# Optimization experiments

Measured on AMD Instinct MI355X. Metric: run time of the kernel, lower is better.

## Reference

```python
import jax, jax.numpy as jnp
import numpy as np
import math

B, T, C = 2, 2048, 1024
N_HEADS = 16  # config.head_size in the original (actually number of heads)
HEAD_DIM = C // N_HEADS


def setup_inputs() -> dict:
    key = jax.random.key(0)
    k1, k2, k3 = jax.random.split(key, 3)
    s = 1.0 / math.sqrt(C)
    return {
        "x": jax.random.normal(k1, (B, T, C), dtype=jnp.float32),
        "W_attn": jax.random.normal(k2, (C, 3 * C), dtype=jnp.float32) * s,
        "b_attn": jnp.zeros((3 * C,), dtype=jnp.float32),
        "W_proj": jax.random.normal(k3, (C, C), dtype=jnp.float32) * s,
        "b_proj": jnp.zeros((C,), dtype=jnp.float32),
    }


def reference(x, W_attn, b_attn, W_proj, b_proj):
    Bsz, Tlen, Cdim = x.shape
    qkv = x @ W_attn + b_attn                      # [B,T,3C]
    q, k, v = jnp.split(qkv, 3, axis=-1)
    # [B,T,C] -> [B,H,T,D]
    def to_heads(t):
        return t.reshape(Bsz, Tlen, N_HEADS, HEAD_DIM).transpose(0, 2, 1, 3)
    q, k, v = to_heads(q), to_heads(k), to_heads(v)
    # NOTE: original multiplies by sqrt(head_dim) (faithful to source, not 1/sqrt)
    scale = jnp.asarray(math.sqrt(HEAD_DIM), dtype=x.dtype)
    att = jnp.einsum("bhqd,bhkd->bhqk", q, k) * scale
    causal = jnp.tril(jnp.ones((Tlen, Tlen), dtype=bool))
    att = jnp.where(causal[None, None, :, :], att, jnp.asarray(-jnp.inf, x.dtype))
    att = jax.nn.softmax(att, axis=-1)
    # dropout layers are identity in eval mode
    y = jnp.einsum("bhqk,bhkd->bhqd", att, v)
    y = y.transpose(0, 2, 1, 3).reshape(Bsz, Tlen, Cdim)
    return y @ W_proj + b_proj
```

## Files before the change

### kernel.cpp

```cpp
#include <hip/hip_runtime.h>
#include <hip/hip_bf16.h>


#define B_  2
#define T_  2048
#define C_  1024
#define H_  16
#define D_  64
#define M_  (B_ * T_)
#define N3_ (3 * C_)

typedef __attribute__((ext_vector_type(8))) short s16x8;
typedef __attribute__((ext_vector_type(4))) short s16x4;
typedef __attribute__((ext_vector_type(4))) float f32x4;

typedef const __attribute__((address_space(1))) unsigned int gu32_t;
typedef __attribute__((address_space(3))) unsigned int lu32_t;

#define MFMA16(a, b, c) __builtin_amdgcn_mfma_f32_16x16x32_bf16(a, b, c, 0, 0, 0)

__device__ __forceinline__ void gload_lds16(const short* g, short* l) {
    __builtin_amdgcn_global_load_lds((gu32_t*)g, (lu32_t*)l, 16, 0, 0);
}

__device__ __forceinline__ float b2f(unsigned short u) {
    return __uint_as_float(((unsigned)u) << 16);
}
__device__ __forceinline__ unsigned short f2b(float f) {
    unsigned u = __float_as_uint(f);
    return (unsigned short)((u + 0x7FFFu + ((u >> 16) & 1u)) >> 16);
}
__device__ __forceinline__ float fexp2(float x) {
#if __has_builtin(__builtin_amdgcn_exp2f)
    return __builtin_amdgcn_exp2f(x);
#else
    return exp2f(x);
#endif
}

__global__ __launch_bounds__(256) void cvt_all(
    const float* __restrict__ x,  short* __restrict__ xh,   short* __restrict__ xl,
    const float* __restrict__ Wa, short* __restrict__ WaTh, short* __restrict__ WaTl,
    const float* __restrict__ Wp, short* __restrict__ WpT)
{
    __shared__ short th[64][80];
    __shared__ short tl[64][80];
    const int tid = threadIdx.x;
    const int bid = blockIdx.x;

    if (bid < 2048) {
        int i = (bid * 256 + tid) * 8;
        float4 a = *(const float4*)&x[i];
        float4 b = *(const float4*)&x[i + 4];
        float v[8] = {a.x, a.y, a.z, a.w, b.x, b.y, b.z, b.w};
        s16x8 h, l;
        #pragma unroll
        for (int j = 0; j < 8; j++) {
            unsigned short hb = f2b(v[j]);
            h[j] = (short)hb;
            l[j] = (short)f2b(v[j] - b2f(hb));
        }
        *(s16x8*)&xh[i] = h;
        *(s16x8*)&xl[i] = l;
        return;
    }

    if (bid < 2816) {
        int r  = bid - 2048;
        int bx = r % 48, by = r / 48;
        const int k0 = by * 64, n0 = bx * 64;
        const int R = C_, Cn = N3_;
        {
            int rl = tid >> 4, cl = (tid & 15) * 4;
            #pragma unroll
            for (int i = 0; i < 4; i++) {
                int kr = rl + i * 16;
                float4 v4 = *(const float4*)&Wa[(size_t)(k0 + kr) * Cn + n0 + cl];
                float v[4] = {v4.x, v4.y, v4.z, v4.w};
                #pragma unroll
                for (int j = 0; j < 4; j++) {
                    unsigned short hb = f2b(v[j]);
                    th[cl + j][kr] = (short)hb;
                    tl[cl + j][kr] = (short)f2b(v[j] - b2f(hb));
                }
            }
        }
        __syncthreads();
        {
            int ro = tid >> 2, co = (tid & 3) * 16;
            *(s16x8*)&WaTh[(size_t)(n0 + ro) * R + k0 + co]     = *(s16x8*)&th[ro][co];
            *(s16x8*)&WaTh[(size_t)(n0 + ro) * R + k0 + co + 8] = *(s16x8*)&th[ro][co + 8];
            *(s16x8*)&WaTl[(size_t)(n0 + ro) * R + k0 + co]     = *(s16x8*)&tl[ro][co];
            *(s16x8*)&WaTl[(size_t)(n0 + ro) * R + k0 + co + 8] = *(s16x8*)&tl[ro][co + 8];
        }
        return;
    }

    {
        int r  = bid - 2816;
        int bx = r & 15, by = r >> 4;
        const int k0 = by * 64, n0 = bx * 64;
        const int R = C_, Cn = C_;
        {
            int rl = tid >> 4, cl = (tid & 15) * 4;
            #pragma unroll
            for (int i = 0; i < 4; i++) {
                int kr = rl + i * 16;
                float4 v = *(const float4*)&Wp[(size_t)(k0 + kr) * Cn + n0 + cl];
                th[cl + 0][kr] = (short)f2b(v.x);
                th[cl + 1][kr] = (short)f2b(v.y);
                th[cl + 2][kr] = (short)f2b(v.z);
                th[cl + 3][kr] = (short)f2b(v.w);
            }
        }
        __syncthreads();
        {
            int ro = tid >> 2, co = (tid & 3) * 16;
            *(s16x8*)&WpT[(size_t)(n0 + ro) * R + k0 + co]     = *(s16x8*)&th[ro][co];
            *(s16x8*)&WpT[(size_t)(n0 + ro) * R + k0 + co + 8] = *(s16x8*)&th[ro][co + 8];
        }
    }
}

__global__ __launch_bounds__(256) void qkv_qk(
    const short* __restrict__ Ah, const short* __restrict__ Al,
    const short* __restrict__ BTh, const short* __restrict__ BTl,
    const float* __restrict__ bias,
    short* __restrict__ Qh, short* __restrict__ Ql,
    short* __restrict__ Kh, short* __restrict__ Kl)
{
    __shared__ short Ash[2][128 * 32], Asl[2][128 * 32];
    __shared__ short Bsh[2][128 * 32], Bsl[2][128 * 32];

    const int tid  = threadIdx.x;
    const int wave = tid >> 6, lane = tid & 63;
    const int wm = wave >> 1, wn = wave & 1;
    const int lm = lane & 15, lq = lane >> 4;
    const int fid = blockIdx.y * 16 + blockIdx.x;
    const int wg  = (fid & 7) * 64 + (fid >> 3);
    const int n0  = (wg & 15) * 128;
    const int m0  = (wg >> 4) * 128;
    const int gr  = (lane >> 2);
    const int gc  = (((lane & 3) ^ ((lane >> 3) & 3)) << 3);
    const int sg  = ((lq ^ ((lm >> 1) & 3)) << 3);

    f32x4 acc[4][4] = {};

    for (int k0 = 0; k0 < C_; k0 += 64) {
        __syncthreads();
        #pragma unroll
        for (int p = 0; p < 2; p++) {
            int kp = k0 + p * 32;
            #pragma unroll
            for (int j = 0; j < 2; j++) {
                int s = wave * 2 + j;
                int row = s * 16 + gr;
                size_t ga = (size_t)(m0 + row) * C_ + kp + gc;
                size_t gb = (size_t)(n0 + row) * C_ + kp + gc;
                gload_lds16(&Ah[ga],  &Ash[p][s * 512]);
                gload_lds16(&Al[ga],  &Asl[p][s * 512]);
                gload_lds16(&BTh[gb], &Bsh[p][s * 512]);
                gload_lds16(&BTl[gb], &Bsl[p][s * 512]);
            }
        }
        __syncthreads();

        #pragma unroll
        for (int p = 0; p < 2; p++) {
            s16x8 ah[4], al[4], bh[4], bl[4];
            #pragma unroll
            for (int mi = 0; mi < 4; mi++) {
                int r = wm * 64 + mi * 16 + lm;
                ah[mi] = *(const s16x8*)&Ash[p][r * 32 + sg];
                al[mi] = *(const s16x8*)&Asl[p][r * 32 + sg];
            }
            #pragma unroll
            for (int nj = 0; nj < 4; nj++) {
                int r = wn * 64 + nj * 16 + lm;
                bh[nj] = *(const s16x8*)&Bsh[p][r * 32 + sg];
                bl[nj] = *(const s16x8*)&Bsl[p][r * 32 + sg];
            }
            #pragma unroll
            for (int mi = 0; mi < 4; mi++)
                #pragma unroll
                for (int nj = 0; nj < 4; nj++) {
                    acc[mi][nj] = MFMA16(ah[mi], bh[nj], acc[mi][nj]);
                    acc[mi][nj] = MFMA16(ah[mi], bl[nj], acc[mi][nj]);
                    acc[mi][nj] = MFMA16(al[mi], bh[nj], acc[mi][nj]);
                }
        }
    }

    #pragma unroll
    for (int nj = 0; nj < 4; nj++) {
        int n = n0 + wn * 64 + nj * 16 + lm;
        float bv = bias[n];
        int isK = n >> 10;
        int c = n & (C_ - 1);
        int h = c >> 6, d = c & (D_ - 1);
        short* dh = isK ? Kh : Qh;
        short* dl = isK ? Kl : Ql;
        float scale = isK ? 1.0f : 11.541560327111708f;
        #pragma unroll
        for (int mi = 0; mi < 4; mi++) {
            #pragma unroll
            for (int r = 0; r < 4; r++) {
                int m  = m0 + wm * 64 + mi * 16 + lq * 4 + r;
                int bb = m >> 11, t = m & (T_ - 1);
                float v = (acc[mi][nj][r] + bv) * scale;
                size_t idx = (((size_t)bb * H_ + h) * T_ + t) * D_ + d;
                unsigned short hb = f2b(v);
                dh[idx] = (short)hb;
                dl[idx] = (short)f2b(v - b2f(hb));
            }
        }
    }
}

__global__ __launch_bounds__(256, 4) void qkv_v(
    const short* __restrict__ Ah, const short* __restrict__ BTh,
    const float* __restrict__ bias, short* __restrict__ VT)
{
    __shared__ short Ash[2][64 * 32];
    __shared__ short Bsh[2][128 * 32];

    const int tid  = threadIdx.x;
    const int wave = tid >> 6, lane = tid & 63;
    const int wm = wave >> 1, wn = wave & 1;
    const int lm = lane & 15, lq = lane >> 4;
    const int fid = blockIdx.y * 8 + blockIdx.x;
    const int wg  = (fid & 7) * 64 + (fid >> 3);
    const int n0  = (wg & 7) * 128;
    const int m0  = (wg >> 3) * 64;
    const int gr  = (lane >> 2);
    const int gc  = (((lane & 3) ^ ((lane >> 3) & 3)) << 3);
    const int sg  = ((lq ^ ((lm >> 1) & 3)) << 3);

    f32x4 acc[2][4] = {};

    for (int k0 = 0; k0 < C_; k0 += 64) {
        __syncthreads();
        #pragma unroll
        for (int p = 0; p < 2; p++) {
            int kp = k0 + p * 32;
            int rowA = wave * 16 + gr;
            gload_lds16(&Ah[(size_t)(m0 + rowA) * C_ + kp + gc], &Ash[p][wave * 512]);
            #pragma unroll
            for (int j = 0; j < 2; j++) {
                int s = wave * 2 + j;
                int rowB = s * 16 + gr;
                gload_lds16(&BTh[(size_t)(n0 + rowB) * C_ + kp + gc], &Bsh[p][s * 512]);
            }
        }
        __syncthreads();

        #pragma unroll
        for (int p = 0; p < 2; p++) {
            s16x8 af[2], bfr[4];
            #pragma unroll
            for (int mi = 0; mi < 2; mi++)
                af[mi] = *(const s16x8*)&Ash[p][(wm * 32 + mi * 16 + lm) * 32 + sg];
            #pragma unroll
            for (int nj = 0; nj < 4; nj++)
                bfr[nj] = *(const s16x8*)&Bsh[p][(wn * 64 + nj * 16 + lm) * 32 + sg];
            #pragma unroll
            for (int mi = 0; mi < 2; mi++)
                #pragma unroll
                for (int nj = 0; nj < 4; nj++)
                    acc[mi][nj] = MFMA16(af[mi], bfr[nj], acc[mi][nj]);
        }
    }

    #pragma unroll
    for (int nj = 0; nj < 4; nj++) {
        int n = n0 + wn * 64 + nj * 16 + lm;
        float bv = bias[n];
        int h = n >> 6, d = n & (D_ - 1);
        #pragma unroll
        for (int mi = 0; mi < 2; mi++) {
            #pragma unroll
            for (int r = 0; r < 4; r++) {
                int m  = m0 + wm * 32 + mi * 16 + lq * 4 + r;
                int bb = m >> 11, t = m & (T_ - 1);
                VT[(((size_t)bb * H_ + h) * D_ + d) * T_ + t] =
                    (short)f2b(acc[mi][nj][r] + bv);
            }
        }
    }
}

__global__ __launch_bounds__(256, 4) void proj_mfma(
    const short* __restrict__ Ah, const short* __restrict__ BTh,
    const float* __restrict__ bias, float* __restrict__ out)
{
    __shared__ short Ash[2][64 * 32];
    __shared__ short Bsh[2][128 * 32];

    const int tid  = threadIdx.x;
    const int wave = tid >> 6, lane = tid & 63;
    const int wm = wave >> 1, wn = wave & 1;
    const int lm = lane & 15, lq = lane >> 4;
    const int fid = blockIdx.y * 8 + blockIdx.x;
    const int wg  = (fid & 7) * 64 + (fid >> 3);
    const int n0  = (wg & 7) * 128;
    const int m0  = (wg >> 3) * 64;
    const int gr  = (lane >> 2);
    const int gc  = (((lane & 3) ^ ((lane >> 3) & 3)) << 3);
    const int sg  = ((lq ^ ((lm >> 1) & 3)) << 3);

    f32x4 acc[2][4] = {};

    for (int k0 = 0; k0 < C_; k0 += 64) {
        __syncthreads();
        #pragma unroll
        for (int p = 0; p < 2; p++) {
            int kp = k0 + p * 32;
            int rowA = wave * 16 + gr;
            gload_lds16(&Ah[(size_t)(m0 + rowA) * C_ + kp + gc], &Ash[p][wave * 512]);
            #pragma unroll
            for (int j = 0; j < 2; j++) {
                int s = wave * 2 + j;
                int rowB = s * 16 + gr;
                gload_lds16(&BTh[(size_t)(n0 + rowB) * C_ + kp + gc], &Bsh[p][s * 512]);
            }
        }
        __syncthreads();

        #pragma unroll
        for (int p = 0; p < 2; p++) {
            s16x8 af[2], bfr[4];
            #pragma unroll
            for (int mi = 0; mi < 2; mi++)
                af[mi] = *(const s16x8*)&Ash[p][(wm * 32 + mi * 16 + lm) * 32 + sg];
            #pragma unroll
            for (int nj = 0; nj < 4; nj++)
                bfr[nj] = *(const s16x8*)&Bsh[p][(wn * 64 + nj * 16 + lm) * 32 + sg];
            #pragma unroll
            for (int mi = 0; mi < 2; mi++)
                #pragma unroll
                for (int nj = 0; nj < 4; nj++)
                    acc[mi][nj] = MFMA16(af[mi], bfr[nj], acc[mi][nj]);
        }
    }

    #pragma unroll
    for (int nj = 0; nj < 4; nj++) {
        int n = n0 + wn * 64 + nj * 16 + lm;
        float bv = bias[n];
        #pragma unroll
        for (int mi = 0; mi < 2; mi++) {
            #pragma unroll
            for (int r = 0; r < 4; r++) {
                int m = m0 + wm * 32 + mi * 16 + lq * 4 + r;
                out[(size_t)m * C_ + n] = acc[mi][nj][r] + bv;
            }
        }
    }
}

__device__ __forceinline__ void online_sm(
    f32x4 S[4], float& mrow, float& lrow, f32x4 O[4], int quad)
{
    float v[16];
    #pragma unroll
    for (int t = 0; t < 4; t++)
        #pragma unroll
        for (int r = 0; r < 4; r++) v[t * 4 + r] = S[t][r];
    #pragma unroll
    for (int s = 8; s; s >>= 1)
        #pragma unroll
        for (int i = 0; i < s; i++) v[i] = fmaxf(v[i], v[i + s]);
    float rm = v[0];
    rm = fmaxf(rm, __shfl_xor(rm, 16, 64));
    rm = fmaxf(rm, __shfl_xor(rm, 32, 64));
    if (!__all(rm - mrow <= 8.f)) {
        float mnew  = fmaxf(mrow, rm);
        float alpha = fexp2(mrow - mnew);
        mrow = mnew;
        lrow *= alpha;
        float al[4];
        #pragma unroll
        for (int r = 0; r < 4; r++) al[r] = __shfl(alpha, quad * 4 + r, 64);
        #pragma unroll
        for (int t = 0; t < 4; t++)
            #pragma unroll
            for (int r = 0; r < 4; r++) O[t][r] *= al[r];
    }
    float sv[16];
    #pragma unroll
    for (int t = 0; t < 4; t++)
        #pragma unroll
        for (int r = 0; r < 4; r++) {
            float p = fexp2(S[t][r] - mrow);
            S[t][r] = p;
            sv[t * 4 + r] = p;
        }
    #pragma unroll
    for (int s = 8; s; s >>= 1)
        #pragma unroll
        for (int i = 0; i < s; i++) sv[i] += sv[i + s];
    float rs = sv[0];
    rs += __shfl_xor(rs, 16, 64);
    rs += __shfl_xor(rs, 32, 64);
    lrow += rs;
}

__global__ __launch_bounds__(256, 2) void attn_mfma(
    const short* __restrict__ Qh, const short* __restrict__ Ql,
    const short* __restrict__ Kh, const short* __restrict__ Kl,
    const short* __restrict__ VT, short* __restrict__ Yb)
{
    __shared__ short Ksh[64][64], Ksl[64][64];
    __shared__ short Vt [64][64];
    __shared__ short Ps [4][2][16][64];

    const int tid  = threadIdx.x;
    const int wave = tid >> 6, lane = tid & 63;
    const int lm   = lane & 15, quad = lane >> 4;
    const int swz  = (lm & 7) << 3;

    const int bid = blockIdx.x;
    const int xcd = bid & 7;
    const int r_  = bid >> 3;
    const int bhl = r_ & 3;
    const int u   = r_ >> 2;
    const int g_  = u >> 3, j_ = u & 7;
    const int j   = g_ ? (15 - j_) : j_;
    const int bh  = xcd * 4 + bhl;
    const int b   = bh >> 4, h = bh & (H_ - 1);
    const int qtA = j, qtB = 31 - j;
    const int q0A = qtA * 64, q0B = qtB * 64;
    const size_t base  = (size_t)bh * T_ * D_;
    const size_t vbase = (size_t)bh * D_ * T_;

    const int src = tid >> 3;
    const int sch = (tid & 7) * 8;
    const int wsw = sch ^ ((src & 7) << 3);

    s16x8 bqhA[2], bqlA[2], bqhB[2], bqlB[2];
    #pragma unroll
    for (int kc = 0; kc < 2; kc++) {
        size_t ga = base + (size_t)(q0A + wave * 16 + lm) * D_ + kc * 32 + quad * 8;
        size_t gb = base + (size_t)(q0B + wave * 16 + lm) * D_ + kc * 32 + quad * 8;
        bqhA[kc] = *(const s16x8*)&Qh[ga];
        bqlA[kc] = *(const s16x8*)&Ql[ga];
        bqhB[kc] = *(const s16x8*)&Qh[gb];
        bqlB[kc] = *(const s16x8*)&Ql[gb];
    }

    s16x8 pkh[2], pkl[2], pvt[2];
    #pragma unroll
    for (int i = 0; i < 2; i++) {
        int row = i * 32 + src;
        size_t gk = base + (size_t)row * D_ + sch;
        pkh[i] = *(const s16x8*)&Kh[gk];
        pkl[i] = *(const s16x8*)&Kl[gk];
        pvt[i] = *(const s16x8*)&VT[vbase + (size_t)row * T_ + sch];
    }

    float mA = -INFINITY, lA = 0.f;
    float mB = -INFINITY, lB = 0.f;
    f32x4 OA[4] = {}, OB[4] = {};

    for (int kt = 0; kt <= qtB; kt++) {
        __syncthreads();
        #pragma unroll
        for (int i = 0; i < 2; i++) {
            int row = i * 32 + src;
            *(s16x8*)&Ksh[row][wsw] = pkh[i];
            *(s16x8*)&Ksl[row][wsw] = pkl[i];
            *(s16x8*)&Vt [row][wsw] = pvt[i];
        }
        if (kt < qtB) {
            #pragma unroll
            for (int i = 0; i < 2; i++) {
                int row = i * 32 + src;
                size_t gk = base + (size_t)((kt + 1) * 64 + row) * D_ + sch;
                pkh[i] = *(const s16x8*)&Kh[gk];
                pkl[i] = *(const s16x8*)&Kl[gk];
                pvt[i] = *(const s16x8*)&VT[vbase + (size_t)row * T_ + (kt + 1) * 64 + sch];
            }
        }
        __syncthreads();

        const bool doA = (kt <= qtA);
        const int  qg  = wave * 16 + lm;

        f32x4 SB[4] = {}, SA[4] = {};
        if (doA) {
            #pragma unroll
            for (int t = 0; t < 4; t++)
                #pragma unroll
                for (int kc = 0; kc < 2; kc++) {
                    s16x8 kh8 = *(const s16x8*)&Ksh[t * 16 + lm][(kc * 32 + quad * 8) ^ swz];
                    s16x8 kl8 = *(const s16x8*)&Ksl[t * 16 + lm][(kc * 32 + quad * 8) ^ swz];
                    SB[t] = MFMA16(kh8, bqhB[kc], SB[t]);
                    SB[t] = MFMA16(kl8, bqhB[kc], SB[t]);
                    SB[t] = MFMA16(kh8, bqlB[kc], SB[t]);
                    SA[t] = MFMA16(kh8, bqhA[kc], SA[t]);
                    SA[t] = MFMA16(kl8, bqhA[kc], SA[t]);
                    SA[t] = MFMA16(kh8, bqlA[kc], SA[t]);
                }
        } else {
            #pragma unroll
            for (int t = 0; t < 4; t++)
                #pragma unroll
                for (int kc = 0; kc < 2; kc++) {
                    s16x8 kh8 = *(const s16x8*)&Ksh[t * 16 + lm][(kc * 32 + quad * 8) ^ swz];
                    s16x8 kl8 = *(const s16x8*)&Ksl[t * 16 + lm][(kc * 32 + quad * 8) ^ swz];
                    SB[t] = MFMA16(kh8, bqhB[kc], SB[t]);
                    SB[t] = MFMA16(kl8, bqhB[kc], SB[t]);
                    SB[t] = MFMA16(kh8, bqlB[kc], SB[t]);
                }
        }

        if (kt == qtB) {
            #pragma unroll
            for (int t = 0; t < 4; t++)
                #pragma unroll
                for (int r = 0; r < 4; r++)
                    if ((t * 16 + quad * 4 + r) > qg) SB[t][r] = -INFINITY;
        }
        if (kt == qtA) {
            #pragma unroll
            for (int t = 0; t < 4; t++)
                #pragma unroll
                for (int r = 0; r < 4; r++)
                    if ((t * 16 + quad * 4 + r) > qg) SA[t][r] = -INFINITY;
        }

        online_sm(SB, mB, lB, OB, quad);
        if (doA) online_sm(SA, mA, lA, OA, quad);

        #pragma unroll
        for (int t = 0; t < 4; t++) {
            s16x4 p;
            #pragma unroll
            for (int r = 0; r < 4; r++)
                p[r] = (short)(__float_as_uint(SB[t][r]) >> 16);
            *(s16x4*)&Ps[wave][0][lm][(t * 16 + quad * 4) ^ swz] = p;
        }
        if (doA) {
            #pragma unroll
            for (int t = 0; t < 4; t++) {
                s16x4 p;
                #pragma unroll
                for (int r = 0; r < 4; r++)
                    p[r] = (short)(__float_as_uint(SA[t][r]) >> 16);
                *(s16x4*)&Ps[wave][1][lm][(t * 16 + quad * 4) ^ swz] = p;
            }
        }

        s16x8 apB[2], apA[2];
        #pragma unroll
        for (int kc = 0; kc < 2; kc++)
            apB[kc] = *(const s16x8*)&Ps[wave][0][lm][(kc * 32 + quad * 8) ^ swz];
        if (doA) {
            #pragma unroll
            for (int kc = 0; kc < 2; kc++)
                apA[kc] = *(const s16x8*)&Ps[wave][1][lm][(kc * 32 + quad * 8) ^ swz];
            #pragma unroll
            for (int t = 0; t < 4; t++)
                #pragma unroll
                for (int kc = 0; kc < 2; kc++) {
                    s16x8 bv = *(const s16x8*)&Vt[t * 16 + lm][(kc * 32 + quad * 8) ^ swz];
                    OB[t] = MFMA16(apB[kc], bv, OB[t]);
                    OA[t] = MFMA16(apA[kc], bv, OA[t]);
                }
        } else {
            #pragma unroll
            for (int t = 0; t < 4; t++)
                #pragma unroll
                for (int kc = 0; kc < 2; kc++) {
                    s16x8 bv = *(const s16x8*)&Vt[t * 16 + lm][(kc * 32 + quad * 8) ^ swz];
                    OB[t] = MFMA16(apB[kc], bv, OB[t]);
                }
        }
    }

    float liA[4], liB[4];
    #pragma unroll
    for (int r = 0; r < 4; r++) {
        liA[r] = 1.0f / __shfl(lA, quad * 4 + r, 64);
        liB[r] = 1.0f / __shfl(lB, quad * 4 + r, 64);
    }
    #pragma unroll
    for (int t = 0; t < 4; t++)
        #pragma unroll
        for (int r = 0; r < 4; r++) {
            int d  = t * 16 + lm;
            int qa = q0A + wave * 16 + quad * 4 + r;
            int qb = q0B + wave * 16 + quad * 4 + r;
            Yb[((size_t)b * T_ + qa) * C_ + h * D_ + d] =
                (short)f2b(OA[t][r] * liA[r]);
            Yb[((size_t)b * T_ + qb) * C_ + h * D_ + d] =
                (short)f2b(OB[t][r] * liB[r]);
        }
}

extern "C" void kernel_launch(void* const* d_in, const int* in_sizes, int n_in,
                              void* d_out, int out_size, void* d_ws, size_t ws_size,
                              hipStream_t stream)
{
    const float* x      = (const float*)d_in[0];
    const float* W_attn = (const float*)d_in[1];
    const float* b_attn = (const float*)d_in[2];
    const float* W_proj = (const float*)d_in[3];
    const float* b_proj = (const float*)d_in[4];
    float* out = (float*)d_out;

    char* ws = (char*)d_ws;
    const size_t MB = 1024 * 1024;
    short* Qh   = (short*)(ws);
    short* Ql   = (short*)(ws +  8 * MB);
    short* Kh   = (short*)(ws + 16 * MB);
    short* Kl   = (short*)(ws + 24 * MB);
    short* xh   = (short*)(ws + 32 * MB);
    short* xl   = (short*)(ws + 40 * MB);
    short* WaTh = (short*)(ws + 48 * MB);
    short* WaTl = (short*)(ws + 54 * MB);
    short* WpT  = (short*)(ws + 60 * MB);
    short* VT   = (short*)(ws + 40 * MB);
    short* Yb   = (short*)(ws + 32 * MB);

    cvt_all<<<dim3(3072), 256, 0, stream>>>(x, xh, xl, W_attn, WaTh, WaTl,
                                            W_proj, WpT);

    qkv_qk <<<dim3(16, 32), 256, 0, stream>>>(xh, xl, WaTh, WaTl, b_attn,
                                              Qh, Ql, Kh, Kl);
    qkv_v  <<<dim3(8, 64), 256, 0, stream>>>(xh, WaTh + (size_t)2048 * C_,
                                             b_attn + 2048, VT);
    attn_mfma<<<dim3(512), 256, 0, stream>>>(Qh, Ql, Kh, Kl, VT, Yb);
    proj_mfma<<<dim3(8, 64), 256, 0, stream>>>(Yb, WpT, b_proj, out);
}
```

Before: 239.5 us.

## Double attention key tile to 128 keys per iteration

Each loop iteration of the attention kernel now processes 128 keys instead of 64. The K, K-low and V tiles in shared memory are enlarged to match, and the causal mask uses a half-tile threshold. This halves the loop trips, barriers and online-softmax rescale checks. In exchange it uses more LDS and registers, which may lower occupancy, and it computes extra masked work on the diagonal chunk when the query tile index is even.

```diff
diff --git a/kernel.cpp b/kernel.cpp
--- a/kernel.cpp
+++ b/kernel.cpp
@@ -358,19 +358,18 @@
     }
 }
 
-__device__ __forceinline__ void online_sm(
-    f32x4 S[4], float& mrow, float& lrow, f32x4 O[4], int quad)
+__device__ __forceinline__ void online_sm8(
+    f32x4 S[8], float& mrow, float& lrow, f32x4 O[4], int quad)
 {
-    float v[16];
-    #pragma unroll
-    for (int t = 0; t < 4; t++)
-        #pragma unroll
-        for (int r = 0; r < 4; r++) v[t * 4 + r] = S[t][r];
-    #pragma unroll
-    for (int s = 8; s; s >>= 1)
-        #pragma unroll
-        for (int i = 0; i < s; i++) v[i] = fmaxf(v[i], v[i + s]);
-    float rm = v[0];
+    float a[8];
+    #pragma unroll
+    for (int t = 0; t < 8; t++)
+        a[t] = fmaxf(fmaxf(S[t][0], S[t][1]), fmaxf(S[t][2], S[t][3]));
+    #pragma unroll
+    for (int s = 4; s; s >>= 1)
+        #pragma unroll
+        for (int i = 0; i < s; i++) a[i] = fmaxf(a[i], a[i + s]);
+    float rm = a[0];
     rm = fmaxf(rm, __shfl_xor(rm, 16, 64));
     rm = fmaxf(rm, __shfl_xor(rm, 32, 64));
     if (!__all(rm - mrow <= 8.f)) {
@@ -386,17 +385,15 @@
             #pragma unroll
             for (int r = 0; r < 4; r++) O[t][r] *= al[r];
     }
-    float sv[16];
-    #pragma unroll
-    for (int t = 0; t < 4; t++)
-        #pragma unroll
-        for (int r = 0; r < 4; r++) {
-            float p = fexp2(S[t][r] - mrow);
-            S[t][r] = p;
-            sv[t * 4 + r] = p;
-        }
-    #pragma unroll
-    for (int s = 8; s; s >>= 1)
+    float sv[8];
+    #pragma unroll
+    for (int t = 0; t < 8; t++) {
+        #pragma unroll
+        for (int r = 0; r < 4; r++) S[t][r] = fexp2(S[t][r] - mrow);
+        sv[t] = (S[t][0] + S[t][1]) + (S[t][2] + S[t][3]);
+    }
+    #pragma unroll
+    for (int s = 4; s; s >>= 1)
         #pragma unroll
         for (int i = 0; i < s; i++) sv[i] += sv[i + s];
     float rs = sv[0];
@@ -410,9 +407,9 @@
     const short* __restrict__ Kh, const short* __restrict__ Kl,
     const short* __restrict__ VT, short* __restrict__ Yb)
 {
-    __shared__ short Ksh[64][64], Ksl[64][64];
-    __shared__ short Vt [64][64];
-    __shared__ short Ps [4][2][16][64];
+    __shared__ short Ksh[128][64], Ksl[128][64];
+    __shared__ short Vt [64][128];
+    __shared__ short Ps [4][2][16][128];
 
     const int tid  = threadIdx.x;
     const int wave = tid >> 6, lane = tid & 63;
@@ -430,12 +427,11 @@
     const int b   = bh >> 4, h = bh & (H_ - 1);
     const int qtA = j, qtB = 31 - j;
     const int q0A = qtA * 64, q0B = qtB * 64;
+    const int cA  = qtA >> 1, cB = qtB >> 1;
+    const int thrA = (qtA & 1) << 6;
+    const int thrB = (qtB & 1) << 6;
     const size_t base  = (size_t)bh * T_ * D_;
     const size_t vbase = (size_t)bh * D_ * T_;
-
-    const int src = tid >> 3;
-    const int sch = (tid & 7) * 8;
-    const int wsw = sch ^ ((src & 7) << 3);
 
     s16x8 bqhA[2], bqlA[2], bqhB[2], bqlB[2];
     #pragma unroll
@@ -448,48 +444,56 @@
         bqlB[kc] = *(const s16x8*)&Ql[gb];
     }
 
-    s16x8 pkh[2], pkl[2], pvt[2];
-    #pragma unroll
-    for (int i = 0; i < 2; i++) {
-        int row = i * 32 + src;
-        size_t gk = base + (size_t)row * D_ + sch;
+    s16x8 pkh[4], pkl[4], pvt[4];
+    #pragma unroll
+    for (int i = 0; i < 4; i++) {
+        int g  = i * 256 + tid;
+        int rk = g >> 3, ck = (g & 7) * 8;
+        size_t gk = base + (size_t)rk * D_ + ck;
         pkh[i] = *(const s16x8*)&Kh[gk];
         pkl[i] = *(const s16x8*)&Kl[gk];
-        pvt[i] = *(const s16x8*)&VT[vbase + (size_t)row * T_ + sch];
+        int rv = g >> 4, cv = (g & 15) * 8;
+        pvt[i] = *(const s16x8*)&VT[vbase + (size_t)rv * T_ + cv];
     }
 
     float mA = -INFINITY, lA = 0.f;
     float mB = -INFINITY, lB = 0.f;
     f32x4 OA[4] = {}, OB[4] = {};
 
-    for (int kt = 0; kt <= qtB; kt++) {
-        __syncthreads();
-        #pragma unroll
-        for (int i = 0; i < 2; i++) {
-            int row = i * 32 + src;
-            *(s16x8*)&Ksh[row][wsw] = pkh[i];
-            *(s16x8*)&Ksl[row][wsw] = pkl[i];
-            *(s16x8*)&Vt [row][wsw] = pvt[i];
-        }
-        if (kt < qtB) {
-            #pragma unroll
-            for (int i = 0; i < 2; i++) {
-                int row = i * 32 + src;
-                size_t gk = base + (size_t)((kt + 1) * 64 + row) * D_ + sch;
+    for (int c = 0; c <= cB; c++) {
+        __syncthreads();
+        #pragma unroll
+        for (int i = 0; i < 4; i++) {
+            int g  = i * 256 + tid;
+            int rk = g >> 3;
+            int wK = ((g & 7) * 8) ^ ((rk & 7) << 3);
+            *(s16x8*)&Ksh[rk][wK] = pkh[i];
+            *(s16x8*)&Ksl[rk][wK] = pkl[i];
+            int rv = g >> 4;
+            int wV = ((g & 15) * 8) ^ ((rv & 7) << 3);
+            *(s16x8*)&Vt[rv][wV] = pvt[i];
+        }
+        if (c < cB) {
+            #pragma unroll
+            for (int i = 0; i < 4; i++) {
+                int g  = i * 256 + tid;
+                int rk = g >> 3, ck = (g & 7) * 8;
+                size_t gk = base + (size_t)((c + 1) * 128 + rk) * D_ + ck;
                 pkh[i] = *(const s16x8*)&Kh[gk];
                 pkl[i] = *(const s16x8*)&Kl[gk];
-                pvt[i] = *(const s16x8*)&VT[vbase + (size_t)row * T_ + (kt + 1) * 64 + sch];
-            }
-        }
-        __syncthreads();
-
-        const bool doA = (kt <= qtA);
+                int rv = g >> 4, cv = (g & 15) * 8;
+                pvt[i] = *(const s16x8*)&VT[vbase + (size_t)rv * T_ + (c + 1) * 128 + cv];
+            }
+        }
+        __syncthreads();
+
+        const bool doA = (c <= cA);
         const int  qg  = wave * 16 + lm;
 
-        f32x4 SB[4] = {}, SA[4] = {};
+        f32x4 SB[8] = {}, SA[8] = {};
         if (doA) {
             #pragma unroll
-            for (int t = 0; t < 4; t++)
+            for (int t = 0; t < 8; t++)
                 #pragma unroll
                 for (int kc = 0; kc < 2; kc++) {
                     s16x8 kh8 = *(const s16x8*)&Ksh[t * 16 + lm][(kc * 32 + quad * 8) ^ swz];
@@ -503,7 +507,7 @@
                 }
         } else {
             #pragma unroll
-            for (int t = 0; t < 4; t++)
+            for (int t = 0; t < 8; t++)
                 #pragma unroll
                 for (int kc = 0; kc < 2; kc++) {
                     s16x8 kh8 = *(const s16x8*)&Ksh[t * 16 + lm][(kc * 32 + quad * 8) ^ swz];
@@ -514,26 +518,26 @@
                 }
         }
 
-        if (kt == qtB) {
-            #pragma unroll
-            for (int t = 0; t < 4; t++)
+        if (c == cB) {
+            #pragma unroll
+            for (int t = 0; t < 8; t++)
                 #pragma unroll
                 for (int r = 0; r < 4; r++)
-                    if ((t * 16 + quad * 4 + r) > qg) SB[t][r] = -INFINITY;
-        }
-        if (kt == qtA) {
-            #pragma unroll
-            for (int t = 0; t < 4; t++)
+                    if ((t * 16 + quad * 4 + r) > thrB + qg) SB[t][r] = -INFINITY;
+        }
+        if (c == cA) {
+            #pragma unroll
+            for (int t = 0; t < 8; t++)
                 #pragma unroll
                 for (int r = 0; r < 4; r++)
-                    if ((t * 16 + quad * 4 + r) > qg) SA[t][r] = -INFINITY;
-        }
-
-        online_sm(SB, mB, lB, OB, quad);
-        if (doA) online_sm(SA, mA, lA, OA, quad);
-
-        #pragma unroll
-        for (int t = 0; t < 4; t++) {
+                    if ((t * 16 + quad * 4 + r) > thrA + qg) SA[t][r] = -INFINITY;
+        }
+
+        online_sm8(SB, mB, lB, OB, quad);
+        if (doA) online_sm8(SA, mA, lA, OA, quad);
+
+        #pragma unroll
+        for (int t = 0; t < 8; t++) {
             s16x4 p;
             #pragma unroll
             for (int r = 0; r < 4; r++)
@@ -542,7 +546,7 @@
         }
         if (doA) {
             #pragma unroll
-            for (int t = 0; t < 4; t++) {
+            for (int t = 0; t < 8; t++) {
                 s16x4 p;
                 #pragma unroll
                 for (int r = 0; r < 4; r++)
@@ -551,18 +555,18 @@
             }
         }
 
-        s16x8 apB[2], apA[2];
-        #pragma unroll
-        for (int kc = 0; kc < 2; kc++)
+        s16x8 apB[4], apA[4];
+        #pragma unroll
+        for (int kc = 0; kc < 4; kc++)
             apB[kc] = *(const s16x8*)&Ps[wave][0][lm][(kc * 32 + quad * 8) ^ swz];
         if (doA) {
             #pragma unroll
-            for (int kc = 0; kc < 2; kc++)
+            for (int kc = 0; kc < 4; kc++)
                 apA[kc] = *(const s16x8*)&Ps[wave][1][lm][(kc * 32 + quad * 8) ^ swz];
             #pragma unroll
             for (int t = 0; t < 4; t++)
                 #pragma unroll
-                for (int kc = 0; kc < 2; kc++) {
+                for (int kc = 0; kc < 4; kc++) {
                     s16x8 bv = *(const s16x8*)&Vt[t * 16 + lm][(kc * 32 + quad * 8) ^ swz];
                     OB[t] = MFMA16(apB[kc], bv, OB[t]);
                     OA[t] = MFMA16(apA[kc], bv, OA[t]);
@@ -571,7 +575,7 @@
             #pragma unroll
             for (int t = 0; t < 4; t++)
                 #pragma unroll
-                for (int kc = 0; kc < 2; kc++) {
+                for (int kc = 0; kc < 4; kc++) {
                     s16x8 bv = *(const s16x8*)&Vt[t * 16 + lm][(kc * 32 + quad * 8) ^ swz];
                     OB[t] = MFMA16(apB[kc], bv, OB[t]);
                 }
```

Result: slower. 246.8 us (+3.0%).
